# Kernel tuning notes

Hardware: AMD Instinct MI355X
Metric: run time of the kernel (lower is better)

Reference implementation:

```python
import jax, jax.numpy as jnp
import numpy as np

B, T, C = 2, 2048, 1024
N_HEAD, D_HEAD = 16, 64


def setup_inputs() -> dict:
    key = jax.random.key(0)
    k1, k2, k3 = jax.random.split(key, 3)
    scale_in = 1.0 / np.sqrt(C)
    return {
        "x": jax.random.normal(k1, (B, T, C), dtype=jnp.float32),
        "W_attn": jax.random.normal(k2, (C, 3 * C), dtype=jnp.float32) * scale_in,
        "b_attn": jnp.zeros((3 * C,), dtype=jnp.float32),
        "W_proj": jax.random.normal(k3, (C, C), dtype=jnp.float32) * scale_in,
        "b_proj": jnp.zeros((C,), dtype=jnp.float32),
    }


def reference(x, W_attn, b_attn, W_proj, b_proj):
    Bx, Tx, Cx = x.shape
    qkv = x @ W_attn + b_attn                       # [B,T,3C]
    q, k, v = jnp.split(qkv, 3, axis=-1)
    # [B,T,C] -> [B,H,T,Dh]
    q = q.reshape(Bx, Tx, N_HEAD, D_HEAD).transpose(0, 2, 1, 3)
    k = k.reshape(Bx, Tx, N_HEAD, D_HEAD).transpose(0, 2, 1, 3)
    v = v.reshape(Bx, Tx, N_HEAD, D_HEAD).transpose(0, 2, 1, 3)
    att = jnp.einsum("bhqd,bhkd->bhqk", q, k) * (1.0 / jnp.sqrt(D_HEAD))
    causal_mask = jnp.tril(jnp.ones((Tx, Tx), dtype=jnp.bool_))[None, None]
    att = jnp.where(causal_mask, att, -jnp.inf)
    att = jax.nn.softmax(att, axis=-1)
    y = jnp.einsum("bhqk,bhkd->bhqd", att, v)        # [B,H,T,Dh]
    y = y.transpose(0, 2, 1, 3).reshape(Bx, Tx, Cx)  # [B,T,C]
    return y @ W_proj + b_proj
```

## Files before the change

### kernel.cpp

```cpp
#include <hip/hip_runtime.h>

#define BB 2
#define TT 2048
#define CC 1024
#define NHEAD 16
#define DHEAD 64

typedef __attribute__((ext_vector_type(8))) short short8;
typedef __attribute__((ext_vector_type(8))) unsigned short ushort8;
typedef __attribute__((ext_vector_type(4))) float floatx4;
typedef __attribute__((ext_vector_type(2))) unsigned int uintx2;

__device__ inline unsigned short f32_to_bf16_rne(float f) {
  unsigned u = __builtin_bit_cast(unsigned, f);
  unsigned r = (u + 0x7FFFu + ((u >> 16) & 1u)) >> 16;
  return (unsigned short)r;
}
__device__ inline unsigned cvt_pk_bf16(float lo, float hi) {
  unsigned r;
  asm("v_cvt_pk_bf16_f32 %0, %1, %2" : "=v"(r) : "v"(lo), "v"(hi));
  return r;
}
__device__ inline void gload_lds16(const void* g, void* l) {
  __builtin_amdgcn_global_load_lds(
      (const __attribute__((address_space(1))) void*)g,
      (__attribute__((address_space(3))) void*)l, 16, 0, 0);
}

__device__ inline void transpose_tile(const float* __restrict__ W,
                                      unsigned short* __restrict__ Wt,
                                      int K, int N, int scale_cut, float scl,
                                      int bx, int by, float (*T)[33]) {
  const int tx = threadIdx.x & 31;
  const int ty = threadIdx.x >> 5;
  const int r0 = by * 32, c0 = bx * 32;
#pragma unroll
  for (int i = 0; i < 4; ++i)
    T[ty + i * 8][tx] = W[(size_t)(r0 + ty + i * 8) * N + c0 + tx];
  __syncthreads();
#pragma unroll
  for (int i = 0; i < 4; ++i) {
    const int nrow = c0 + ty + i * 8;
    const float s = (nrow < scale_cut) ? scl : 1.0f;
    Wt[(size_t)nrow * K + r0 + tx] = f32_to_bf16_rne(T[tx][ty + i * 8] * s);
  }
}

__global__ __launch_bounds__(256) void prep_kernel(
    const float* __restrict__ x, const float* __restrict__ W_attn,
    const float* __restrict__ b_attn, const float* __restrict__ W_proj,
    unsigned short* __restrict__ xb, unsigned short* __restrict__ Wat,
    unsigned short* __restrict__ Wpt, float* __restrict__ bscl, float scl) {
  __shared__ float T[32][33];
  const int id = blockIdx.x;
  if (id < 4096) {
    const int i = (id * 256 + threadIdx.x) * 4;
    float4 v = *(const float4*)(x + i);
    ushort4 o;
    o.x = f32_to_bf16_rne(v.x);
    o.y = f32_to_bf16_rne(v.y);
    o.z = f32_to_bf16_rne(v.z);
    o.w = f32_to_bf16_rne(v.w);
    *(ushort4*)(xb + i) = o;
  } else if (id < 4096 + 3072) {
    const int t = id - 4096;
    transpose_tile(W_attn, Wat, CC, 3 * CC, CC, scl, t % 96, t / 96, T);
  } else if (id < 4096 + 3072 + 1024) {
    const int t = id - (4096 + 3072);
    transpose_tile(W_proj, Wpt, CC, CC, 0, 1.0f, t % 32, t / 32, T);
  } else {
    const int i = (id - 8192) * 256 + threadIdx.x;
    if (i < 3 * CC) bscl[i] = b_attn[i] * (i < CC ? scl : 1.0f);
  }
}

__global__ __launch_bounds__(256) void transpose_v_kernel(
    const unsigned short* __restrict__ qkv, unsigned short* __restrict__ vT) {
  __shared__ unsigned short Ts[64][72];
  const int tt0 = blockIdx.x * 64;
  const int bh = blockIdx.y;
  const int h = bh & (NHEAD - 1);
  const int b = bh >> 4;
  const int tid = threadIdx.x;
  const unsigned short* src = qkv + (size_t)(b * TT) * (3 * CC) + 2 * CC + h * DHEAD;
#pragma unroll
  for (int it = 0; it < 2; ++it) {
    const int t = it * 32 + (tid >> 3);
    const int d8 = (tid & 7) * 8;
    ushort8 v = *(const ushort8*)(src + (size_t)(tt0 + t) * (3 * CC) + d8);
#pragma unroll
    for (int j = 0; j < 8; ++j) Ts[t][d8 + j] = v[j];
  }
  __syncthreads();
  unsigned short* dst = vT + ((size_t)((b * NHEAD + h) * DHEAD)) * TT;
#pragma unroll
  for (int it = 0; it < 2; ++it) {
    const int d = it * 32 + (tid >> 3);
    const int t8 = (tid & 7) * 8;
    ushort8 o;
#pragma unroll
    for (int j = 0; j < 8; ++j) o[j] = Ts[t8 + j][d];
    *(ushort8*)(dst + (size_t)d * TT + tt0 + t8) = o;
  }
}

template <bool BF16_OUT, int BN>
__global__ __launch_bounds__(256) void gemm_mfma_kernel(
    const unsigned short* __restrict__ A, const unsigned short* __restrict__ Bt,
    const float* __restrict__ bias, void* __restrict__ Cout,
    int M, int N, int K) {
  constexpr int NR = BN / 32;
  __shared__ unsigned short As[128 * 32];
  __shared__ unsigned short Bs[BN * 32];

  const int tid = threadIdx.x;
  const int wave = tid >> 6;
  const int lane = tid & 63;
  const int row0 = blockIdx.y * 128;
  const int col0 = blockIdx.x * BN;
  const int wr = (wave >> 1) * 64;
  const int wc = (wave & 1) * (BN / 2);

  floatx4 acc[4][NR];
#pragma unroll
  for (int m = 0; m < 4; ++m)
#pragma unroll
    for (int n = 0; n < NR; ++n) acc[m][n] = (floatx4){0.f, 0.f, 0.f, 0.f};

  const int sRow = lane >> 2;
  const int sK = (lane & 3) * 8;

  for (int k0 = 0; k0 < K; k0 += 32) {
#pragma unroll
    for (int c = 0; c < 2; ++c) {
      const int g = c * 4 + wave;
      gload_lds16(A + (size_t)(row0 + g * 16 + sRow) * K + k0 + sK,
                  (char*)As + g * 1024);
    }
    if constexpr (BN == 128) {
#pragma unroll
      for (int c = 0; c < 2; ++c) {
        const int g = c * 4 + wave;
        gload_lds16(Bt + (size_t)(col0 + g * 16 + sRow) * K + k0 + sK,
                    (char*)Bs + g * 1024);
      }
    } else {
      gload_lds16(Bt + (size_t)(col0 + wave * 16 + sRow) * K + k0 + sK,
                  (char*)Bs + wave * 1024);
    }
    __syncthreads();

    short8 af[4], bf[NR];
#pragma unroll
    for (int m = 0; m < 4; ++m)
      af[m] = *(const short8*)(As + (wr + m * 16 + (lane & 15)) * 32 + (lane >> 4) * 8);
#pragma unroll
    for (int n = 0; n < NR; ++n)
      bf[n] = *(const short8*)(Bs + (wc + n * 16 + (lane & 15)) * 32 + (lane >> 4) * 8);
#pragma unroll
    for (int m = 0; m < 4; ++m)
#pragma unroll
      for (int n = 0; n < NR; ++n)
        acc[m][n] = __builtin_amdgcn_mfma_f32_16x16x32_bf16(af[m], bf[n], acc[m][n], 0, 0, 0);
    __syncthreads();
  }

  const int cl = lane & 15;
  const int rg = (lane >> 4) * 4;
#pragma unroll
  for (int m = 0; m < 4; ++m) {
#pragma unroll
    for (int n = 0; n < NR; ++n) {
      const int col = col0 + wc + n * 16 + cl;
      const float bv = bias[col];
#pragma unroll
      for (int r = 0; r < 4; ++r) {
        const int row = row0 + wr + m * 16 + rg + r;
        const float v = acc[m][n][r] + bv;
        if (BF16_OUT)
          ((unsigned short*)Cout)[(size_t)row * N + col] = f32_to_bf16_rne(v);
        else
          ((float*)Cout)[(size_t)row * N + col] = v;
      }
    }
  }
}

__global__ __launch_bounds__(256) void flash_mfma_kernel(
    const unsigned short* __restrict__ qkv,
    const unsigned short* __restrict__ vT,
    unsigned short* __restrict__ y) {
  __shared__ unsigned short Ks[64 * 64];
  __shared__ unsigned short Vs[64 * 64];
  __shared__ unsigned short Ps[4][16 * 64];

  const int id = blockIdx.x;
  const int xcd = id & 7;
  const int k = id >> 3;
  const int grp = k >> 5;
  const int j = k & 31;
  const int base = (j & 1) ? (j >> 1) : (31 - (j >> 1));
  const int qt = (grp & 1) ? (31 - base) : base;
  const int bh = xcd * 4 + grp;

  const int h = bh & (NHEAD - 1);
  const int b = bh >> 4;
  const int tid = threadIdx.x;
  const int wq = tid >> 6;
  const int lane = tid & 63;
  const int l15 = lane & 15;
  const int l4 = lane >> 4;
  const int srow = lane >> 3;
  const int schunk = lane & 7;

  const int qminw = qt * 64 + wq * 16;

  const size_t baseQ = (size_t)(b * TT) * (3 * CC) + h * DHEAD;
  const size_t baseK = baseQ + CC;
  const size_t vbase = (size_t)((b * NHEAD + h) * DHEAD) * TT;

  short8 aq[2];
  {
    const unsigned short* qp =
        qkv + baseQ + (size_t)(qminw + l15) * (3 * CC) + l4 * 8;
    aq[0] = *(const short8*)(qp);
    aq[1] = *(const short8*)(qp + 32);
  }

  floatx4 accT[4];
  float m_i = -1e30f, l_i = 0.f;
#pragma unroll
  for (int n = 0; n < 4; ++n) accT[n] = (floatx4){0.f, 0.f, 0.f, 0.f};

  const int nt = qt + 1;

  for (int kt = 0; kt < nt; ++kt) {
    if (kt) __builtin_amdgcn_s_barrier();

#pragma unroll
    for (int it = 0; it < 2; ++it) {
      const int blk = it * 4 + wq;
      const int grow = blk * 8 + srow;
      gload_lds16(qkv + baseK + (size_t)(kt * 64 + grow) * (3 * CC) +
                      (schunk ^ srow) * 8,
                  (char*)Ks + blk * 1024);
      gload_lds16(vT + vbase + (size_t)grow * TT + kt * 64 + (schunk ^ srow) * 8,
                  (char*)Vs + blk * 1024);
    }
    asm volatile("s_waitcnt vmcnt(0)" ::: "memory");
    __builtin_amdgcn_s_barrier();

    floatx4 sa[4];
#pragma unroll
    for (int f = 0; f < 4; ++f) sa[f] = (floatx4){0.f, 0.f, 0.f, 0.f};

    __builtin_amdgcn_s_setprio(1);
#pragma unroll
    for (int kc = 0; kc < 2; ++kc) {
#pragma unroll
      for (int f = 0; f < 4; ++f) {
        const int row = 16 * f + l15;
        short8 bk = *(const short8*)(Ks + row * 64 +
                                     ((kc * 4 + l4) ^ (row & 7)) * 8);
        sa[f] = __builtin_amdgcn_mfma_f32_16x16x32_bf16(bk, aq[kc], sa[f], 0, 0, 0);
      }
    }
    __builtin_amdgcn_s_setprio(0);

    const int qg = qminw + l15;
    if (kt * 64 + 63 > qminw) {
#pragma unroll
      for (int f = 0; f < 4; ++f)
#pragma unroll
        for (int r = 0; r < 4; ++r) {
          const int kg = kt * 64 + f * 16 + l4 * 4 + r;
          if (kg > qg) sa[f][r] = -1e30f;
        }
    }
    float rm = -1e30f;
#pragma unroll
    for (int f = 0; f < 4; ++f)
      rm = fmaxf(rm, fmaxf(fmaxf(sa[f][0], sa[f][1]), fmaxf(sa[f][2], sa[f][3])));
    rm = fmaxf(rm, __shfl_xor(rm, 16, 64));
    rm = fmaxf(rm, __shfl_xor(rm, 32, 64));

    float rs = 0.f;
    if (__all(rm <= m_i + 8.0f)) {
#pragma unroll
      for (int f = 0; f < 4; ++f)
#pragma unroll
        for (int r = 0; r < 4; ++r) {
          const float p = __builtin_amdgcn_exp2f(sa[f][r] - m_i);
          sa[f][r] = p;
          rs += p;
        }
      rs += __shfl_xor(rs, 16, 64);
      rs += __shfl_xor(rs, 32, 64);
      l_i += rs;
    } else {
      const float mn = fmaxf(m_i, rm);
      const float scale = __builtin_amdgcn_exp2f(m_i - mn);
#pragma unroll
      for (int f = 0; f < 4; ++f)
#pragma unroll
        for (int r = 0; r < 4; ++r) {
          const float p = __builtin_amdgcn_exp2f(sa[f][r] - mn);
          sa[f][r] = p;
          rs += p;
        }
      rs += __shfl_xor(rs, 16, 64);
      rs += __shfl_xor(rs, 32, 64);
      l_i = l_i * scale + rs;
      m_i = mn;
#pragma unroll
      for (int nd = 0; nd < 4; ++nd) accT[nd] *= scale;
    }

    char* Pg = (char*)Ps[wq];
#pragma unroll
    for (int f = 0; f < 4; ++f) {
      uintx2 dw;
      dw[0] = cvt_pk_bf16(sa[f][0], sa[f][1]);
      dw[1] = cvt_pk_bf16(sa[f][2], sa[f][3]);
      const int c = f * 2 + (l4 >> 1);
      *(uintx2*)(Pg + l15 * 128 + ((c ^ (l15 & 7)) * 16) + (l4 & 1) * 8) = dw;
    }
    asm volatile("s_waitcnt lgkmcnt(0)" ::: "memory");

    short8 pb[2];
#pragma unroll
    for (int kc = 0; kc < 2; ++kc) {
      const int c = kc * 4 + l4;
      pb[kc] = *(const short8*)(Pg + l15 * 128 + ((c ^ (l15 & 7)) * 16));
    }

    __builtin_amdgcn_s_setprio(1);
#pragma unroll
    for (int kc = 0; kc < 2; ++kc) {
#pragma unroll
      for (int nd = 0; nd < 4; ++nd) {
        const int row = 16 * nd + l15;
        short8 vb = *(const short8*)(Vs + row * 64 +
                                     ((kc * 4 + l4) ^ (row & 7)) * 8);
        accT[nd] = __builtin_amdgcn_mfma_f32_16x16x32_bf16(vb, pb[kc], accT[nd], 0, 0, 0);
      }
    }
    __builtin_amdgcn_s_setprio(0);
  }

  char* Pw = (char*)Ps[wq];
  {
    const float inv = 1.0f / l_i;
#pragma unroll
    for (int nd = 0; nd < 4; ++nd) {
      uintx2 dw;
      dw[0] = cvt_pk_bf16(accT[nd][0] * inv, accT[nd][1] * inv);
      dw[1] = cvt_pk_bf16(accT[nd][2] * inv, accT[nd][3] * inv);
      const int c = nd * 2 + (l4 >> 1);
      *(uintx2*)(Pw + l15 * 128 + ((c ^ (l15 & 7)) * 16) + (l4 & 1) * 8) = dw;
    }
  }
  asm volatile("s_waitcnt lgkmcnt(0)" ::: "memory");
#pragma unroll
  for (int ch = 0; ch < 2; ++ch) {
    const int q16 = lane >> 2;
    const int c = ch * 4 + (lane & 3);
    ushort8 o = *(const ushort8*)(Pw + q16 * 128 + ((c ^ (q16 & 7)) * 16));
    const int qg = qt * 64 + wq * 16 + q16;
    *(ushort8*)(y + (size_t)(b * TT + qg) * CC + h * DHEAD + c * 8) = o;
  }
}

extern "C" void kernel_launch(void* const* d_in, const int* in_sizes, int n_in,
                              void* d_out, int out_size, void* d_ws, size_t ws_size,
                              hipStream_t stream) {
  const float* x      = (const float*)d_in[0];
  const float* W_attn = (const float*)d_in[1];
  const float* b_attn = (const float*)d_in[2];
  const float* W_proj = (const float*)d_in[3];
  const float* b_proj = (const float*)d_in[4];
  float* out = (float*)d_out;

  const int M = BB * TT;
  const float SCL = 0.125f * 1.44269504089f;

  unsigned short* qkvb = (unsigned short*)d_ws;
  unsigned short* xb   = qkvb + (size_t)M * 3 * CC;
  unsigned short* Wat  = xb + (size_t)M * CC;
  unsigned short* Wpt  = Wat + (size_t)3 * CC * CC;
  unsigned short* yb   = Wpt + (size_t)CC * CC;
  unsigned short* vTb  = yb + (size_t)M * CC;
  float* bscl = (float*)(vTb + (size_t)BB * NHEAD * DHEAD * TT);

  prep_kernel<<<8204, 256, 0, stream>>>(x, W_attn, b_attn, W_proj,
                                        xb, Wat, Wpt, bscl, SCL);

  {
    dim3 grid((3 * CC) / 128, M / 128);
    gemm_mfma_kernel<true, 128><<<grid, 256, 0, stream>>>(xb, Wat, bscl, qkvb, M, 3 * CC, CC);
  }

  {
    dim3 grid(TT / 64, BB * NHEAD);
    transpose_v_kernel<<<grid, 256, 0, stream>>>(qkvb, vTb);
  }

  flash_mfma_kernel<<<1024, 256, 0, stream>>>(qkvb, vTb, yb);

  {
    dim3 grid(CC / 64, M / 128);
    gemm_mfma_kernel<false, 64><<<grid, 256, 0, stream>>>(yb, Wpt, b_proj, out, M, CC, CC);
  }
}
```

Before: 129.3 us.

## Pair causal query tiles per block and double-buffer K/V loads in flash attention

Each block now processes two query tiles (qt and 31-qt) of the same head in sequence, which balances the causal work and halves the grid to 512 blocks. K/V tiles are double-buffered in LDS, so the next tile's global-to-LDS load is issued before computing on the current one. This aims to hide load latency and remove tail imbalance. In exchange it doubles LDS use and fixes each block to 33 tiles of work, which may reduce occupancy and latency hiding across blocks.

```diff
diff --git a/kernel.cpp b/kernel.cpp
--- a/kernel.cpp
+++ b/kernel.cpp
@@ -190,18 +190,17 @@
     const unsigned short* __restrict__ qkv,
     const unsigned short* __restrict__ vT,
     unsigned short* __restrict__ y) {
-  __shared__ unsigned short Ks[64 * 64];
-  __shared__ unsigned short Vs[64 * 64];
+  __shared__ unsigned short Ks[2][64 * 64];
+  __shared__ unsigned short Vs[2][64 * 64];
   __shared__ unsigned short Ps[4][16 * 64];
 
   const int id = blockIdx.x;
   const int xcd = id & 7;
-  const int k = id >> 3;
-  const int grp = k >> 5;
-  const int j = k & 31;
-  const int base = (j & 1) ? (j >> 1) : (31 - (j >> 1));
-  const int qt = (grp & 1) ? (31 - base) : base;
+  const int grp = (id >> 3) & 3;
+  const int p = id >> 5;
   const int bh = xcd * 4 + grp;
+  const int qtA = 31 - p, qtB = p;
+  const int ntA = qtA + 1, ntB = qtB + 1;
 
   const int h = bh & (NHEAD - 1);
   const int b = bh >> 4;
@@ -213,18 +212,20 @@
   const int srow = lane >> 3;
   const int schunk = lane & 7;
 
-  const int qminw = qt * 64 + wq * 16;
-
   const size_t baseQ = (size_t)(b * TT) * (3 * CC) + h * DHEAD;
   const size_t baseK = baseQ + CC;
   const size_t vbase = (size_t)((b * NHEAD + h) * DHEAD) * TT;
 
-  short8 aq[2];
+  short8 aqA[2], aqB[2];
   {
     const unsigned short* qp =
-        qkv + baseQ + (size_t)(qminw + l15) * (3 * CC) + l4 * 8;
-    aq[0] = *(const short8*)(qp);
-    aq[1] = *(const short8*)(qp + 32);
+        qkv + baseQ + (size_t)(qtA * 64 + wq * 16 + l15) * (3 * CC) + l4 * 8;
+    aqA[0] = *(const short8*)(qp);
+    aqA[1] = *(const short8*)(qp + 32);
+    const unsigned short* qp2 =
+        qkv + baseQ + (size_t)(qtB * 64 + wq * 16 + l15) * (3 * CC) + l4 * 8;
+    aqB[0] = *(const short8*)(qp2);
+    aqB[1] = *(const short8*)(qp2 + 32);
   }
 
   floatx4 accT[4];
@@ -232,23 +233,54 @@
 #pragma unroll
   for (int n = 0; n < 4; ++n) accT[n] = (floatx4){0.f, 0.f, 0.f, 0.f};
 
-  const int nt = qt + 1;
-
-  for (int kt = 0; kt < nt; ++kt) {
-    if (kt) __builtin_amdgcn_s_barrier();
-
+  auto stage = [&](int KT, int BUF) {
 #pragma unroll
     for (int it = 0; it < 2; ++it) {
       const int blk = it * 4 + wq;
       const int grow = blk * 8 + srow;
-      gload_lds16(qkv + baseK + (size_t)(kt * 64 + grow) * (3 * CC) +
+      gload_lds16(qkv + baseK + (size_t)(KT * 64 + grow) * (3 * CC) +
                       (schunk ^ srow) * 8,
-                  (char*)Ks + blk * 1024);
-      gload_lds16(vT + vbase + (size_t)grow * TT + kt * 64 + (schunk ^ srow) * 8,
-                  (char*)Vs + blk * 1024);
-    }
-    asm volatile("s_waitcnt vmcnt(0)" ::: "memory");
-    __builtin_amdgcn_s_barrier();
+                  (char*)Ks[BUF] + blk * 1024);
+      gload_lds16(vT + vbase + (size_t)grow * TT + KT * 64 + (schunk ^ srow) * 8,
+                  (char*)Vs[BUF] + blk * 1024);
+    }
+  };
+
+  auto epilogue = [&](int qt) {
+    char* Pw = (char*)Ps[wq];
+    const float inv = 1.0f / l_i;
+#pragma unroll
+    for (int nd = 0; nd < 4; ++nd) {
+      uintx2 dw;
+      dw[0] = cvt_pk_bf16(accT[nd][0] * inv, accT[nd][1] * inv);
+      dw[1] = cvt_pk_bf16(accT[nd][2] * inv, accT[nd][3] * inv);
+      const int c = nd * 2 + (l4 >> 1);
+      *(uintx2*)(Pw + l15 * 128 + ((c ^ (l15 & 7)) * 16) + (l4 & 1) * 8) = dw;
+    }
+    asm volatile("s_waitcnt lgkmcnt(0)" ::: "memory");
+#pragma unroll
+    for (int ch = 0; ch < 2; ++ch) {
+      const int q16 = lane >> 2;
+      const int c = ch * 4 + (lane & 3);
+      ushort8 o = *(const ushort8*)(Pw + q16 * 128 + ((c ^ (q16 & 7)) * 16));
+      const int qg = qt * 64 + wq * 16 + q16;
+      *(ushort8*)(y + (size_t)(b * TT + qg) * CC + h * DHEAD + c * 8) = o;
+    }
+  };
+
+  const int nt_total = ntA + ntB;
+
+  stage(0, 0);
+  asm volatile("s_waitcnt vmcnt(0)" ::: "memory");
+  __builtin_amdgcn_s_barrier();
+
+  for (int t = 0; t < nt_total; ++t) {
+    const bool phB = (t >= ntA);
+    const int kt = phB ? t - ntA : t;
+    const int qminw = (phB ? qtB : qtA) * 64 + wq * 16;
+    const int cur = t & 1;
+    if (t + 1 < nt_total)
+      stage((t + 1 >= ntA) ? t + 1 - ntA : t + 1, cur ^ 1);
 
     floatx4 sa[4];
 #pragma unroll
@@ -257,12 +289,13 @@
     __builtin_amdgcn_s_setprio(1);
 #pragma unroll
     for (int kc = 0; kc < 2; ++kc) {
+      const short8 aq = phB ? aqB[kc] : aqA[kc];
 #pragma unroll
       for (int f = 0; f < 4; ++f) {
         const int row = 16 * f + l15;
-        short8 bk = *(const short8*)(Ks + row * 64 +
+        short8 bk = *(const short8*)(Ks[cur] + row * 64 +
                                      ((kc * 4 + l4) ^ (row & 7)) * 8);
-        sa[f] = __builtin_amdgcn_mfma_f32_16x16x32_bf16(bk, aq[kc], sa[f], 0, 0, 0);
+        sa[f] = __builtin_amdgcn_mfma_f32_16x16x32_bf16(bk, aq, sa[f], 0, 0, 0);
       }
     }
     __builtin_amdgcn_s_setprio(0);
@@ -290,9 +323,9 @@
       for (int f = 0; f < 4; ++f)
 #pragma unroll
         for (int r = 0; r < 4; ++r) {
-          const float p = __builtin_amdgcn_exp2f(sa[f][r] - m_i);
-          sa[f][r] = p;
-          rs += p;
+          const float pv = __builtin_amdgcn_exp2f(sa[f][r] - m_i);
+          sa[f][r] = pv;
+          rs += pv;
         }
       rs += __shfl_xor(rs, 16, 64);
       rs += __shfl_xor(rs, 32, 64);
@@ -304,9 +337,9 @@
       for (int f = 0; f < 4; ++f)
 #pragma unroll
         for (int r = 0; r < 4; ++r) {
-          const float p = __builtin_amdgcn_exp2f(sa[f][r] - mn);
-          sa[f][r] = p;
-          rs += p;
+          const float pv = __builtin_amdgcn_exp2f(sa[f][r] - mn);
+          sa[f][r] = pv;
+          rs += pv;
         }
       rs += __shfl_xor(rs, 16, 64);
       rs += __shfl_xor(rs, 32, 64);
@@ -340,35 +373,26 @@
 #pragma unroll
       for (int nd = 0; nd < 4; ++nd) {
         const int row = 16 * nd + l15;
-        short8 vb = *(const short8*)(Vs + row * 64 +
+        short8 vb = *(const short8*)(Vs[cur] + row * 64 +
                                      ((kc * 4 + l4) ^ (row & 7)) * 8);
         accT[nd] = __builtin_amdgcn_mfma_f32_16x16x32_bf16(vb, pb[kc], accT[nd], 0, 0, 0);
       }
     }
     __builtin_amdgcn_s_setprio(0);
-  }
-
-  char* Pw = (char*)Ps[wq];
-  {
-    const float inv = 1.0f / l_i;
-#pragma unroll
-    for (int nd = 0; nd < 4; ++nd) {
-      uintx2 dw;
-      dw[0] = cvt_pk_bf16(accT[nd][0] * inv, accT[nd][1] * inv);
-      dw[1] = cvt_pk_bf16(accT[nd][2] * inv, accT[nd][3] * inv);
-      const int c = nd * 2 + (l4 >> 1);
-      *(uintx2*)(Pw + l15 * 128 + ((c ^ (l15 & 7)) * 16) + (l4 & 1) * 8) = dw;
-    }
-  }
-  asm volatile("s_waitcnt lgkmcnt(0)" ::: "memory");
-#pragma unroll
-  for (int ch = 0; ch < 2; ++ch) {
-    const int q16 = lane >> 2;
-    const int c = ch * 4 + (lane & 3);
-    ushort8 o = *(const ushort8*)(Pw + q16 * 128 + ((c ^ (q16 & 7)) * 16));
-    const int qg = qt * 64 + wq * 16 + q16;
-    *(ushort8*)(y + (size_t)(b * TT + qg) * CC + h * DHEAD + c * 8) = o;
-  }
+
+    asm volatile("s_waitcnt vmcnt(0)" ::: "memory");
+    __builtin_amdgcn_s_barrier();
+
+    if (t == ntA - 1) {
+      epilogue(qtA);
+      m_i = -1e30f;
+      l_i = 0.f;
+#pragma unroll
+      for (int n = 0; n < 4; ++n) accT[n] = (floatx4){0.f, 0.f, 0.f, 0.f};
+    }
+  }
+
+  epilogue(qtB);
 }
 
 extern "C" void kernel_launch(void* const* d_in, const int* in_sizes, int n_in,
@@ -405,7 +429,7 @@
     transpose_v_kernel<<<grid, 256, 0, stream>>>(qkvb, vTb);
   }
 
-  flash_mfma_kernel<<<1024, 256, 0, stream>>>(qkvb, vTb, yb);
+  flash_mfma_kernel<<<512, 256, 0, stream>>>(qkvb, vTb, yb);
 
   {
     dim3 grid(CC / 64, M / 128);
```

After: 123.4 us. 4.6% less time.
